# Performance work log

Hardware: AMD Instinct MI355X
Metric: run time of the kernel (lower is better)

## Reference

```python
import jax, jax.numpy as jnp
import numpy as np

HEADS = 8
HEAD_DIM = 48
INNER = HEADS * HEAD_DIM  # 384
GROUPS = 32
EPS = 1e-5
SCALE = HEAD_DIM ** -0.5


def group_norm(x, w, b):
    # x: [B,C,H,W]; GroupNorm(32, C) as in diffusion-style normalization()
    B, C, H, W = x.shape
    xg = x.reshape(B, GROUPS, C // GROUPS, H, W)
    mu = xg.mean(axis=(2, 3, 4), keepdims=True)
    var = xg.var(axis=(2, 3, 4), keepdims=True)
    xg = (xg - mu) * jax.lax.rsqrt(var + EPS)
    return xg.reshape(B, C, H, W) * w[None, :, None, None] + b[None, :, None, None]


def conv1x1(x, w, b):
    # 1x1 conv == per-pixel linear: w [Cout,Cin], x [B,Cin,H,W]
    return jnp.einsum('oc,bchw->bohw', w, x) + b[None, :, None, None]


def to_heads(t):
    # [B, INNER, H, W] -> [B, heads, H*W, head_dim]
    B, C, H, W = t.shape
    return t.reshape(B, HEADS, HEAD_DIM, H * W).transpose(0, 1, 3, 2)


def setup_inputs() -> dict:
    key = jax.random.key(0)
    ks = jax.random.split(key, 8)
    B, Cq, H, W = 4, 256, 48, 48
    return {
        'q_feat': jax.random.normal(ks[0], (B, Cq, H, W), jnp.float32),
        'kv_feat': jax.random.normal(ks[1], (B, Cq, H, W), jnp.float32),
        'gn_w': jnp.ones((Cq,), jnp.float32),
        'gn_b': jnp.zeros((Cq,), jnp.float32),
        'wq': jax.random.normal(ks[2], (INNER, Cq), jnp.float32) * 0.02,
        'bq': jnp.zeros((INNER,), jnp.float32),
        'wk': jax.random.normal(ks[3], (INNER, Cq), jnp.float32) * 0.02,
        'bk': jnp.zeros((INNER,), jnp.float32),
        'wv': jax.random.normal(ks[4], (INNER, Cq), jnp.float32) * 0.02,
        'bv': jnp.zeros((INNER,), jnp.float32),
        'wo': jax.random.normal(ks[5], (Cq, INNER), jnp.float32) * 0.02,
        'bo': jnp.zeros((Cq,), jnp.float32),
    }


def reference(q_feat, kv_feat, gn_w, gn_b, wq, bq, wk, bk, wv, bv, wo, bo):
    B, Cq, H, W = q_feat.shape
    q = conv1x1(group_norm(q_feat, gn_w, gn_b), wq, bq)
    k = conv1x1(kv_feat, wk, bk)  # kv_norm is Identity
    v = conv1x1(kv_feat, wv, bv)
    qh, kh, vh = to_heads(q), to_heads(k), to_heads(v)  # [B,h,N,d]
    scores = jnp.einsum('bhnd,bhmd->bhnm', qh, kh) * SCALE  # [B,h,N,N]
    attn = jax.nn.softmax(scores, axis=-1)
    o = jnp.einsum('bhnm,bhmd->bhnd', attn, vh)  # [B,h,N,d]
    o = o.transpose(0, 1, 3, 2).reshape(B, INNER, H, W)
    return conv1x1(o, wo, bo) + q_feat
```

## Files before the change

kernel.cpp:

```cpp
#include <hip/hip_runtime.h>
#include <hip/hip_bf16.h>

#define N_PIX 2304
#define C_IN  256
#define INNER 384
#define HEADS 8
#define HDIM  48
#define DPAD  64
#define QSCALE (0.14433756729740643f * 1.44269504088896341f)

typedef __bf16 bf16x8 __attribute__((ext_vector_type(8)));
typedef float  f32x4  __attribute__((ext_vector_type(4)));
typedef short  s16x8  __attribute__((ext_vector_type(8)));

union Frag { s16x8 s; bf16x8 b; uint2 u[2]; };

__device__ inline short f2bf_bits(float f){
  union { float f; unsigned u; } v; v.f = f;
  unsigned r = v.u + 0x7fffu + ((v.u >> 16) & 1u);
  return (short)(r >> 16);
}

__device__ inline unsigned cvt_pk(float a, float b){
  unsigned r; asm("v_cvt_pk_bf16_f32 %0, %1, %2" : "=v"(r) : "v"(a), "v"(b));
  return r;
}

__global__ __launch_bounds__(256) void gn_stats(const float* __restrict__ x,
                                                float* __restrict__ mu,
                                                float* __restrict__ rs){
  int bg = blockIdx.x;
  const float* p = x + (size_t)bg * 8 * N_PIX;
  float s = 0.f, s2 = 0.f;
  for (int i = threadIdx.x; i < 8 * N_PIX; i += 256){
    float v = p[i]; s += v; s2 += v * v;
  }
  __shared__ float ls[256], ls2[256];
  ls[threadIdx.x] = s; ls2[threadIdx.x] = s2;
  __syncthreads();
  for (int off = 128; off > 0; off >>= 1){
    if ((int)threadIdx.x < off){ ls[threadIdx.x] += ls[threadIdx.x + off]; ls2[threadIdx.x] += ls2[threadIdx.x + off]; }
    __syncthreads();
  }
  if (threadIdx.x == 0){
    float m = ls[0] / 18432.f;
    float var = ls2[0] / 18432.f - m * m;
    mu[bg] = m; rs[bg] = rsqrtf(var + 1e-5f);
  }
}

__global__ __launch_bounds__(256) void wconv(const float* __restrict__ a, const float* __restrict__ b,
                                             const float* __restrict__ c, const float* __restrict__ d,
                                             short* __restrict__ dst){
  int i = (blockIdx.x * 256 + threadIdx.x) * 8;
  const float* src;
  if (i < 98304) src = a + i;
  else if (i < 196608) src = b + (i - 98304);
  else if (i < 294912) src = c + (i - 196608);
  else src = d + (i - 294912);
  float4 v0 = *(const float4*)src;
  float4 v1 = *(const float4*)(src + 4);
  uint4 o;
  o.x = cvt_pk(v0.x, v0.y); o.y = cvt_pk(v0.z, v0.w);
  o.z = cvt_pk(v1.x, v1.y); o.w = cvt_pk(v1.z, v1.w);
  *(uint4*)(dst + i) = o;
}

__global__ __launch_bounds__(256) void prep_x(const float* __restrict__ Xq, const float* __restrict__ Xkv,
                                              const float* __restrict__ gnw, const float* __restrict__ gnb,
                                              const float* __restrict__ mu, const float* __restrict__ rs,
                                              short* __restrict__ XTq, short* __restrict__ XTkv){
  int which = blockIdx.z >> 2;
  int b = blockIdx.z & 3;
  int nb = blockIdx.x * 64, cb = blockIdx.y * 64;
  const float* X = which ? Xkv : Xq;
  short* XT = which ? XTkv : XTq;
  __shared__ __align__(16) short lt[64][68];
  int t = threadIdx.x;
  int c_l = t >> 4, n4 = (t & 15) * 4;
  #pragma unroll
  for (int i = 0; i < 4; ++i){
    int cl = c_l + i * 16, c = cb + cl;
    float4 v = *(const float4*)(X + ((size_t)b * C_IN + c) * N_PIX + nb + n4);
    if (which == 0){
      int bg = b * 32 + (c >> 3);
      float w = gnw[c] * rs[bg], bb = gnb[c] - mu[bg] * w;
      v.x = v.x * w + bb; v.y = v.y * w + bb; v.z = v.z * w + bb; v.w = v.w * w + bb;
    }
    uint2 p; p.x = cvt_pk(v.x, v.y); p.y = cvt_pk(v.z, v.w);
    *(uint2*)&lt[cl][n4] = p;
  }
  __syncthreads();
  #pragma unroll
  for (int i = 0; i < 2; ++i){
    int idx = t + i * 256;
    int n = idx >> 3, c8 = (idx & 7) * 8;
    s16x8 o;
    #pragma unroll
    for (int j = 0; j < 8; ++j) o[j] = lt[c8 + j][n];
    *(s16x8*)(XT + ((size_t)b * N_PIX + nb + n) * C_IN + cb + c8) = o;
  }
}

__global__ __launch_bounds__(256) void proj_qk(const short* __restrict__ XT,
                                               const short* __restrict__ WB,
                                               const float* __restrict__ bias,
                                               short* __restrict__ OUT, float scale){
  int b = blockIdx.z, nb = blockIdx.x * 64, ob = blockIdx.y * 64;
  int wave = threadIdx.x >> 6, lane = threadIdx.x & 63;
  int l16 = lane & 15, lq = lane >> 4;
  int o0 = ob + wave * 16;

  f32x4 acc[4] = {};
  const short* xbase = XT + ((size_t)b * N_PIX + nb) * C_IN;
  #pragma unroll
  for (int k = 0; k < 8; ++k){
    Frag wf; wf.s = *(const s16x8*)(WB + (size_t)(o0 + l16) * C_IN + k * 32 + lq * 8);
    #pragma unroll
    for (int nt = 0; nt < 4; ++nt){
      Frag af; af.s = *(const s16x8*)(xbase + (size_t)(nt * 16 + l16) * C_IN + k * 32 + lq * 8);
      acc[nt] = __builtin_amdgcn_mfma_f32_16x16x32_bf16(af.b, wf.b, acc[nt], 0, 0, 0);
    }
  }
  int o = o0 + l16;
  int h = (o * 683) >> 15, d = o - h * 48;
  float bv = bias[o];
  #pragma unroll
  for (int nt = 0; nt < 4; ++nt)
    #pragma unroll
    for (int r = 0; r < 4; ++r){
      int n = nb + nt * 16 + lq * 4 + r;
      OUT[(((size_t)b * HEADS + h) * N_PIX + n) * DPAD + d] = f2bf_bits((acc[nt][r] + bv) * scale);
    }

  if (ob == 0){
    s16x8 z = {0,0,0,0,0,0,0,0};
    for (int i = threadIdx.x; i < 1024; i += 256){
      int n = nb + (i >> 4);
      int hh = (i >> 1) & 7;
      int dd = 48 + (i & 1) * 8;
      *(s16x8*)(OUT + (((size_t)b * HEADS + hh) * N_PIX + n) * DPAD + dd) = z;
    }
  }
}

__global__ __launch_bounds__(256) void proj_v(const short* __restrict__ XT,
                                              const short* __restrict__ WB,
                                              const float* __restrict__ bias,
                                              short* __restrict__ VT){
  int b = blockIdx.z, nb = blockIdx.x * 64, ob = blockIdx.y * 64;
  int wave = threadIdx.x >> 6, lane = threadIdx.x & 63;
  int l16 = lane & 15, lq = lane >> 4;
  int o0 = ob + wave * 16;

  f32x4 acc[4] = {};
  const short* xbase = XT + ((size_t)b * N_PIX + nb) * C_IN;
  #pragma unroll
  for (int k = 0; k < 8; ++k){
    Frag wf; wf.s = *(const s16x8*)(WB + (size_t)(o0 + l16) * C_IN + k * 32 + lq * 8);
    #pragma unroll
    for (int nt = 0; nt < 4; ++nt){
      Frag xf; xf.s = *(const s16x8*)(xbase + (size_t)(nt * 16 + l16) * C_IN + k * 32 + lq * 8);
      acc[nt] = __builtin_amdgcn_mfma_f32_16x16x32_bf16(wf.b, xf.b, acc[nt], 0, 0, 0);
    }
  }
  #pragma unroll
  for (int r = 0; r < 4; ++r){
    int o = o0 + lq * 4 + r;
    int h = (o * 683) >> 15, d = o - h * 48;
    float bv = bias[o];
    #pragma unroll
    for (int nt = 0; nt < 4; ++nt){
      int n = nb + nt * 16 + l16;
      VT[(((size_t)b * HEADS + h) * DPAD + d) * N_PIX + n] = f2bf_bits(acc[nt][r] + bv);
    }
  }
}

__global__ __launch_bounds__(256) void attn_kernel(const short* __restrict__ Q,
                                                   const short* __restrict__ K,
                                                   const short* __restrict__ VT,
                                                   short* __restrict__ AOUT){
  int bh = blockIdx.y;
  int b = bh >> 3, h = bh & 7;
  int ib = blockIdx.x * 64;
  int wave = threadIdx.x >> 6, lane = threadIdx.x & 63;
  int l16 = lane & 15, lq = lane >> 4;
  int q0 = ib + wave * 16;

  __shared__ __align__(16) short kt[64 * 64];
  __shared__ __align__(16) short vt[64 * 64];
  __shared__ __align__(16) short pt[4][16 * 64];

  Frag qf[2];
  {
    const short* qp = Q + ((size_t)bh * N_PIX + q0 + l16) * DPAD + lq * 8;
    qf[0].s = *(const s16x8*)(qp);
    qf[1].s = *(const s16x8*)(qp + 32);
  }

  float m = -1e30f, l = 0.f;
  f32x4 oacc[3] = {};
  short* pw = &pt[wave][0];

  for (int jt = 0; jt < N_PIX / 64; ++jt){
    __syncthreads();
    #pragma unroll
    for (int it = 0; it < 2; ++it){
      int idx = threadIdx.x + it * 256;
      int row = idx >> 3, cb = idx & 7;
      int scb = cb ^ (row & 7);
      *(s16x8*)(kt + row * 64 + scb * 8) =
        *(const s16x8*)(K + ((size_t)bh * N_PIX + jt * 64 + row) * DPAD + cb * 8);
      *(s16x8*)(vt + row * 64 + scb * 8) =
        *(const s16x8*)(VT + ((size_t)bh * DPAD + row) * N_PIX + jt * 64 + cb * 8);
    }
    __syncthreads();

    f32x4 sc[4] = {};
    #pragma unroll
    for (int ct = 0; ct < 4; ++ct){
      int jr = ct * 16 + l16;
      #pragma unroll
      for (int kk = 0; kk < 2; ++kk){
        Frag kf;
        kf.s = *(const s16x8*)(kt + jr * 64 + ((kk * 4 + lq) ^ (jr & 7)) * 8);
        sc[ct] = __builtin_amdgcn_mfma_f32_16x16x32_bf16(kf.b, qf[kk].b, sc[ct], 0, 0, 0);
      }
    }

    float mx = fmaxf(
      fmaxf(fmaxf(fmaxf(sc[0][0], sc[0][1]), fmaxf(sc[0][2], sc[0][3])),
            fmaxf(fmaxf(sc[1][0], sc[1][1]), fmaxf(sc[1][2], sc[1][3]))),
      fmaxf(fmaxf(fmaxf(sc[2][0], sc[2][1]), fmaxf(sc[2][2], sc[2][3])),
            fmaxf(fmaxf(sc[3][0], sc[3][1]), fmaxf(sc[3][2], sc[3][3]))));
    mx = fmaxf(mx, __shfl_xor(mx, 16));
    mx = fmaxf(mx, __shfl_xor(mx, 32));
    float mnew = fmaxf(m, mx);
    float corr = __builtin_amdgcn_exp2f(m - mnew);
    m = mnew;
    float ps = 0.f;
    #pragma unroll
    for (int ct = 0; ct < 4; ++ct)
      #pragma unroll
      for (int r = 0; r < 4; ++r){
        float p = __builtin_amdgcn_exp2f(sc[ct][r] - mnew);
        sc[ct][r] = p; ps += p;
      }
    ps += __shfl_xor(ps, 16);
    ps += __shfl_xor(ps, 32);
    l = l * corr + ps;
    #pragma unroll
    for (int dt = 0; dt < 3; ++dt)
      #pragma unroll
      for (int r = 0; r < 4; ++r) oacc[dt][r] *= corr;

    #pragma unroll
    for (int ct = 0; ct < 4; ++ct){
      uint2 p; p.x = cvt_pk(sc[ct][0], sc[ct][1]); p.y = cvt_pk(sc[ct][2], sc[ct][3]);
      *(uint2*)(pw + l16 * 64 + (((ct * 4 + lq) ^ l16) * 4)) = p;
    }

    #pragma unroll
    for (int kk = 0; kk < 2; ++kk){
      Frag pf;
      pf.u[0] = *(const uint2*)(pw + l16 * 64 + ((((kk * 8 + lq * 2)    ) ^ l16) * 4));
      pf.u[1] = *(const uint2*)(pw + l16 * 64 + ((((kk * 8 + lq * 2) + 1) ^ l16) * 4));
      #pragma unroll
      for (int dt = 0; dt < 3; ++dt){
        int vr = dt * 16 + l16;
        Frag vf;
        vf.s = *(const s16x8*)(vt + vr * 64 + ((kk * 4 + lq) ^ (vr & 7)) * 8);
        oacc[dt] = __builtin_amdgcn_mfma_f32_16x16x32_bf16(vf.b, pf.b, oacc[dt], 0, 0, 0);
      }
    }
  }

  float inv = 1.f / l;
  short* op = AOUT + ((size_t)b * N_PIX + q0 + l16) * INNER + h * HDIM + lq * 4;
  #pragma unroll
  for (int dt = 0; dt < 3; ++dt){
    uint2 w;
    w.x = cvt_pk(oacc[dt][0] * inv, oacc[dt][1] * inv);
    w.y = cvt_pk(oacc[dt][2] * inv, oacc[dt][3] * inv);
    *(uint2*)(op + dt * 16) = w;
  }
}

__global__ __launch_bounds__(256) void proj_o(const short* __restrict__ WOB,
                                              const float* __restrict__ BO,
                                              const short* __restrict__ AOUT,
                                              const float* __restrict__ RES,
                                              float* __restrict__ OUT){
  int b = blockIdx.z, nb = blockIdx.x * 64, ob = blockIdx.y * 64;
  int wave = threadIdx.x >> 6, lane = threadIdx.x & 63;
  int l16 = lane & 15, lq = lane >> 4;
  int o0 = ob + wave * 16;

  f32x4 acc[4] = {};
  const short* abase = AOUT + ((size_t)b * N_PIX + nb) * INNER;
  #pragma unroll
  for (int k = 0; k < 12; ++k){
    Frag wf; wf.s = *(const s16x8*)(WOB + (size_t)(o0 + l16) * INNER + k * 32 + lq * 8);
    #pragma unroll
    for (int nt = 0; nt < 4; ++nt){
      Frag af; af.s = *(const s16x8*)(abase + (size_t)(nt * 16 + l16) * INNER + k * 32 + lq * 8);
      acc[nt] = __builtin_amdgcn_mfma_f32_16x16x32_bf16(wf.b, af.b, acc[nt], 0, 0, 0);
    }
  }
  #pragma unroll
  for (int r = 0; r < 4; ++r){
    int o = o0 + lq * 4 + r;
    float bv = BO[o];
    #pragma unroll
    for (int nt = 0; nt < 4; ++nt){
      int n = nb + nt * 16 + l16;
      size_t idx = ((size_t)b * C_IN + o) * N_PIX + n;
      OUT[idx] = acc[nt][r] + bv + RES[idx];
    }
  }
}

extern "C" void kernel_launch(void* const* d_in, const int* in_sizes, int n_in,
                              void* d_out, int out_size, void* d_ws, size_t ws_size,
                              hipStream_t stream){
  const float* q_feat = (const float*)d_in[0];
  const float* kv_feat= (const float*)d_in[1];
  const float* gn_w   = (const float*)d_in[2];
  const float* gn_b   = (const float*)d_in[3];
  const float* wq     = (const float*)d_in[4];
  const float* bq     = (const float*)d_in[5];
  const float* wk     = (const float*)d_in[6];
  const float* bk     = (const float*)d_in[7];
  const float* wv     = (const float*)d_in[8];
  const float* bv     = (const float*)d_in[9];
  const float* wo     = (const float*)d_in[10];
  const float* bo     = (const float*)d_in[11];
  float* out = (float*)d_out;

  char* ws = (char*)d_ws;
  float* mu = (float*)ws;
  float* rs = (float*)(ws + 512);
  short* wbf  = (short*)(ws + 4096);
  short* xtq  = (short*)(ws + 790528);
  short* xtkv = (short*)(ws + 5509120);
  short* qh   = (short*)(ws + 10227712);
  short* kh   = (short*)(ws + 19664896);
  short* vtb  = (short*)(ws + 29102080);
  short* aout = (short*)(ws + 790528);

  gn_stats<<<128, 256, 0, stream>>>(q_feat, mu, rs);
  wconv<<<192, 256, 0, stream>>>(wq, wk, wv, wo, wbf);
  prep_x<<<dim3(36, 4, 8), 256, 0, stream>>>(q_feat, kv_feat, gn_w, gn_b, mu, rs, xtq, xtkv);

  proj_qk<<<dim3(36, 6, 4), 256, 0, stream>>>(xtq,  wbf,          bq, qh, (float)QSCALE);
  proj_qk<<<dim3(36, 6, 4), 256, 0, stream>>>(xtkv, wbf + 98304,  bk, kh, 1.0f);
  proj_v <<<dim3(36, 6, 4), 256, 0, stream>>>(xtkv, wbf + 196608, bv, vtb);

  attn_kernel<<<dim3(36, 32), 256, 0, stream>>>(qh, kh, vtb, aout);

  proj_o<<<dim3(36, 4, 4), 256, 0, stream>>>(wbf + 294912, bo, aout, q_feat, out);
}
```

Before: 290.6 us.

## Merge launches, double K/V tile size with register prefetch, lazy softmax rescale

Merges gn_stats with wconv and the three QKV projections into single launches to cut launch overhead. The attention kernel now works on 128-key tiles, prefetches the next K/V tile into registers while computing the current one, and remaps blocks so that the 8 heads sharing a batch are scheduled together. It also skips the online-softmax rescale unless the running max grows by more than a threshold. These changes raise LDS and register use per block, which may lower occupancy.

```diff
diff --git a/kernel.cpp b/kernel.cpp
--- a/kernel.cpp
+++ b/kernel.cpp
@@ -26,44 +26,44 @@
   return r;
 }
 
-__global__ __launch_bounds__(256) void gn_stats(const float* __restrict__ x,
-                                                float* __restrict__ mu,
-                                                float* __restrict__ rs){
-  int bg = blockIdx.x;
-  const float* p = x + (size_t)bg * 8 * N_PIX;
-  float s = 0.f, s2 = 0.f;
-  for (int i = threadIdx.x; i < 8 * N_PIX; i += 256){
-    float v = p[i]; s += v; s2 += v * v;
-  }
+__global__ __launch_bounds__(256) void gn_wconv(const float* __restrict__ x,
+                                                float* __restrict__ mu, float* __restrict__ rs,
+                                                const float* __restrict__ wa, const float* __restrict__ wb,
+                                                const float* __restrict__ wc, const float* __restrict__ wd,
+                                                short* __restrict__ dst){
   __shared__ float ls[256], ls2[256];
-  ls[threadIdx.x] = s; ls2[threadIdx.x] = s2;
-  __syncthreads();
-  for (int off = 128; off > 0; off >>= 1){
-    if ((int)threadIdx.x < off){ ls[threadIdx.x] += ls[threadIdx.x + off]; ls2[threadIdx.x] += ls2[threadIdx.x + off]; }
+  if (blockIdx.x < 128){
+    int bg = blockIdx.x;
+    const float* p = x + (size_t)bg * 8 * N_PIX;
+    float s = 0.f, s2 = 0.f;
+    for (int i = threadIdx.x; i < 8 * N_PIX; i += 256){
+      float v = p[i]; s += v; s2 += v * v;
+    }
+    ls[threadIdx.x] = s; ls2[threadIdx.x] = s2;
     __syncthreads();
-  }
-  if (threadIdx.x == 0){
-    float m = ls[0] / 18432.f;
-    float var = ls2[0] / 18432.f - m * m;
-    mu[bg] = m; rs[bg] = rsqrtf(var + 1e-5f);
-  }
-}
-
-__global__ __launch_bounds__(256) void wconv(const float* __restrict__ a, const float* __restrict__ b,
-                                             const float* __restrict__ c, const float* __restrict__ d,
-                                             short* __restrict__ dst){
-  int i = (blockIdx.x * 256 + threadIdx.x) * 8;
-  const float* src;
-  if (i < 98304) src = a + i;
-  else if (i < 196608) src = b + (i - 98304);
-  else if (i < 294912) src = c + (i - 196608);
-  else src = d + (i - 294912);
-  float4 v0 = *(const float4*)src;
-  float4 v1 = *(const float4*)(src + 4);
-  uint4 o;
-  o.x = cvt_pk(v0.x, v0.y); o.y = cvt_pk(v0.z, v0.w);
-  o.z = cvt_pk(v1.x, v1.y); o.w = cvt_pk(v1.z, v1.w);
-  *(uint4*)(dst + i) = o;
+    for (int off = 128; off > 0; off >>= 1){
+      if ((int)threadIdx.x < off){ ls[threadIdx.x] += ls[threadIdx.x + off]; ls2[threadIdx.x] += ls2[threadIdx.x + off]; }
+      __syncthreads();
+    }
+    if (threadIdx.x == 0){
+      float m = ls[0] / 18432.f;
+      float var = ls2[0] / 18432.f - m * m;
+      mu[bg] = m; rs[bg] = rsqrtf(var + 1e-5f);
+    }
+  } else {
+    int i = ((blockIdx.x - 128) * 256 + threadIdx.x) * 8;
+    const float* src;
+    if (i < 98304) src = wa + i;
+    else if (i < 196608) src = wb + (i - 98304);
+    else if (i < 294912) src = wc + (i - 196608);
+    else src = wd + (i - 294912);
+    float4 v0 = *(const float4*)src;
+    float4 v1 = *(const float4*)(src + 4);
+    uint4 o;
+    o.x = cvt_pk(v0.x, v0.y); o.y = cvt_pk(v0.z, v0.w);
+    o.z = cvt_pk(v1.x, v1.y); o.w = cvt_pk(v1.z, v1.w);
+    *(uint4*)(dst + i) = o;
+  }
 }
 
 __global__ __launch_bounds__(256) void prep_x(const float* __restrict__ Xq, const float* __restrict__ Xkv,
@@ -102,11 +102,21 @@
   }
 }
 
-__global__ __launch_bounds__(256) void proj_qk(const short* __restrict__ XT,
-                                               const short* __restrict__ WB,
-                                               const float* __restrict__ bias,
-                                               short* __restrict__ OUT, float scale){
-  int b = blockIdx.z, nb = blockIdx.x * 64, ob = blockIdx.y * 64;
+__global__ __launch_bounds__(256) void proj_qkv(const short* __restrict__ XTq,
+                                                const short* __restrict__ XTkv,
+                                                const short* __restrict__ WBF,
+                                                const float* __restrict__ bq,
+                                                const float* __restrict__ bk,
+                                                const float* __restrict__ bv,
+                                                short* __restrict__ QH,
+                                                short* __restrict__ KH,
+                                                short* __restrict__ VTB){
+  int b = blockIdx.z, nb = blockIdx.x * 64;
+  int y = blockIdx.y;
+  int which = y / 6;
+  int ob = (y % 6) * 64;
+  const short* XT = which ? XTkv : XTq;
+  const short* WB = WBF + which * 98304;
   int wave = threadIdx.x >> 6, lane = threadIdx.x & 63;
   int l16 = lane & 15, lq = lane >> 4;
   int o0 = ob + wave * 16;
@@ -119,60 +129,45 @@
     #pragma unroll
     for (int nt = 0; nt < 4; ++nt){
       Frag af; af.s = *(const s16x8*)(xbase + (size_t)(nt * 16 + l16) * C_IN + k * 32 + lq * 8);
-      acc[nt] = __builtin_amdgcn_mfma_f32_16x16x32_bf16(af.b, wf.b, acc[nt], 0, 0, 0);
-    }
-  }
-  int o = o0 + l16;
-  int h = (o * 683) >> 15, d = o - h * 48;
-  float bv = bias[o];
-  #pragma unroll
-  for (int nt = 0; nt < 4; ++nt)
+      acc[nt] = (which == 2)
+        ? __builtin_amdgcn_mfma_f32_16x16x32_bf16(wf.b, af.b, acc[nt], 0, 0, 0)
+        : __builtin_amdgcn_mfma_f32_16x16x32_bf16(af.b, wf.b, acc[nt], 0, 0, 0);
+  }
+  }
+  if (which == 2){
     #pragma unroll
     for (int r = 0; r < 4; ++r){
-      int n = nb + nt * 16 + lq * 4 + r;
-      OUT[(((size_t)b * HEADS + h) * N_PIX + n) * DPAD + d] = f2bf_bits((acc[nt][r] + bv) * scale);
-    }
-
-  if (ob == 0){
-    s16x8 z = {0,0,0,0,0,0,0,0};
-    for (int i = threadIdx.x; i < 1024; i += 256){
-      int n = nb + (i >> 4);
-      int hh = (i >> 1) & 7;
-      int dd = 48 + (i & 1) * 8;
-      *(s16x8*)(OUT + (((size_t)b * HEADS + hh) * N_PIX + n) * DPAD + dd) = z;
-    }
-  }
-}
-
-__global__ __launch_bounds__(256) void proj_v(const short* __restrict__ XT,
-                                              const short* __restrict__ WB,
-                                              const float* __restrict__ bias,
-                                              short* __restrict__ VT){
-  int b = blockIdx.z, nb = blockIdx.x * 64, ob = blockIdx.y * 64;
-  int wave = threadIdx.x >> 6, lane = threadIdx.x & 63;
-  int l16 = lane & 15, lq = lane >> 4;
-  int o0 = ob + wave * 16;
-
-  f32x4 acc[4] = {};
-  const short* xbase = XT + ((size_t)b * N_PIX + nb) * C_IN;
-  #pragma unroll
-  for (int k = 0; k < 8; ++k){
-    Frag wf; wf.s = *(const s16x8*)(WB + (size_t)(o0 + l16) * C_IN + k * 32 + lq * 8);
-    #pragma unroll
-    for (int nt = 0; nt < 4; ++nt){
-      Frag xf; xf.s = *(const s16x8*)(xbase + (size_t)(nt * 16 + l16) * C_IN + k * 32 + lq * 8);
-      acc[nt] = __builtin_amdgcn_mfma_f32_16x16x32_bf16(wf.b, xf.b, acc[nt], 0, 0, 0);
-    }
-  }
-  #pragma unroll
-  for (int r = 0; r < 4; ++r){
-    int o = o0 + lq * 4 + r;
+      int o = o0 + lq * 4 + r;
+      int h = (o * 683) >> 15, d = o - h * 48;
+      float bvv = bv[o];
+      #pragma unroll
+      for (int nt = 0; nt < 4; ++nt){
+        int n = nb + nt * 16 + l16;
+        VTB[(((size_t)b * HEADS + h) * DPAD + d) * N_PIX + n] = f2bf_bits(acc[nt][r] + bvv);
+      }
+    }
+  } else {
+    short* OUT = which ? KH : QH;
+    const float* bias = which ? bk : bq;
+    float scale = which ? 1.0f : (float)QSCALE;
+    int o = o0 + l16;
     int h = (o * 683) >> 15, d = o - h * 48;
-    float bv = bias[o];
-    #pragma unroll
-    for (int nt = 0; nt < 4; ++nt){
-      int n = nb + nt * 16 + l16;
-      VT[(((size_t)b * HEADS + h) * DPAD + d) * N_PIX + n] = f2bf_bits(acc[nt][r] + bv);
+    float bvv = bias[o];
+    #pragma unroll
+    for (int nt = 0; nt < 4; ++nt)
+      #pragma unroll
+      for (int r = 0; r < 4; ++r){
+        int n = nb + nt * 16 + lq * 4 + r;
+        OUT[(((size_t)b * HEADS + h) * N_PIX + n) * DPAD + d] = f2bf_bits((acc[nt][r] + bvv) * scale);
+      }
+    if (which == 0 && ob == 0){
+      s16x8 z = {0,0,0,0,0,0,0,0};
+      for (int i = threadIdx.x; i < 1024; i += 256){
+        int n = nb + (i >> 4);
+        int hh = (i >> 1) & 7;
+        int dd = 48 + (i & 1) * 8;
+        *(s16x8*)(QH + (((size_t)b * HEADS + hh) * N_PIX + n) * DPAD + dd) = z;
+      }
     }
   }
 }
@@ -181,16 +176,26 @@
                                                    const short* __restrict__ K,
                                                    const short* __restrict__ VT,
                                                    short* __restrict__ AOUT){
-  int bh = blockIdx.y;
+  int f = blockIdx.x;
+  int t = f >> 3;
+  int ib = (t % 36) * 64;
+  int bh = (f & 7) + 8 * (t / 36);
   int b = bh >> 3, h = bh & 7;
-  int ib = blockIdx.x * 64;
-  int wave = threadIdx.x >> 6, lane = threadIdx.x & 63;
+  int tid = threadIdx.x;
+  int wave = tid >> 6, lane = tid & 63;
   int l16 = lane & 15, lq = lane >> 4;
   int q0 = ib + wave * 16;
 
-  __shared__ __align__(16) short kt[64 * 64];
-  __shared__ __align__(16) short vt[64 * 64];
-  __shared__ __align__(16) short pt[4][16 * 64];
+  __shared__ __align__(16) short kt[128 * 64];
+  __shared__ __align__(16) short vt[64 * 128];
+  __shared__ __align__(16) short pt[4][16 * 132];
+
+  int kr = tid >> 3, kc = tid & 7;
+  int ksw = (kc ^ (kr & 7)) * 8;
+  int vr = tid >> 4, vc = tid & 15;
+  int vsw = (vc ^ (vr & 7)) * 8;
+  const short* kbase = K + (size_t)bh * N_PIX * DPAD;
+  const short* vbase = VT + (size_t)bh * DPAD * N_PIX;
 
   Frag qf[2];
   {
@@ -199,27 +204,39 @@
     qf[1].s = *(const s16x8*)(qp + 32);
   }
 
+  Frag kst[4], vst[4];
+  #pragma unroll
+  for (int it = 0; it < 4; ++it){
+    kst[it].s = *(const s16x8*)(kbase + (size_t)(kr + it * 32) * DPAD + kc * 8);
+    vst[it].s = *(const s16x8*)(vbase + (size_t)(vr + it * 16) * N_PIX + vc * 8);
+  }
+
   float m = -1e30f, l = 0.f;
   f32x4 oacc[3] = {};
   short* pw = &pt[wave][0];
 
-  for (int jt = 0; jt < N_PIX / 64; ++jt){
+  for (int jt = 0; jt < N_PIX / 128; ++jt){
     __syncthreads();
     #pragma unroll
-    for (int it = 0; it < 2; ++it){
-      int idx = threadIdx.x + it * 256;
-      int row = idx >> 3, cb = idx & 7;
-      int scb = cb ^ (row & 7);
-      *(s16x8*)(kt + row * 64 + scb * 8) =
-        *(const s16x8*)(K + ((size_t)bh * N_PIX + jt * 64 + row) * DPAD + cb * 8);
-      *(s16x8*)(vt + row * 64 + scb * 8) =
-        *(const s16x8*)(VT + ((size_t)bh * DPAD + row) * N_PIX + jt * 64 + cb * 8);
+    for (int it = 0; it < 4; ++it){
+      *(s16x8*)(kt + (kr + it * 32) * 64 + ksw) = kst[it].s;
+      *(s16x8*)(vt + (vr + it * 16) * 128 + vsw) = vst[it].s;
+    }
+    if (jt < N_PIX / 128 - 1){
+      const short* kb2 = kbase + (size_t)(jt + 1) * 128 * DPAD;
+      const short* vb2 = vbase + (jt + 1) * 128;
+      #pragma unroll
+      for (int it = 0; it < 4; ++it){
+        kst[it].s = *(const s16x8*)(kb2 + (size_t)(kr + it * 32) * DPAD + kc * 8);
+        vst[it].s = *(const s16x8*)(vb2 + (size_t)(vr + it * 16) * N_PIX + vc * 8);
+      }
     }
     __syncthreads();
 
-    f32x4 sc[4] = {};
-    #pragma unroll
-    for (int ct = 0; ct < 4; ++ct){
+    f32x4 sc[8];
+    #pragma unroll
+    for (int ct = 0; ct < 8; ++ct){
+      sc[ct] = (f32x4){0.f, 0.f, 0.f, 0.f};
       int jr = ct * 16 + l16;
       #pragma unroll
       for (int kk = 0; kk < 2; ++kk){
@@ -229,48 +246,51 @@
       }
     }
 
-    float mx = fmaxf(
-      fmaxf(fmaxf(fmaxf(sc[0][0], sc[0][1]), fmaxf(sc[0][2], sc[0][3])),
-            fmaxf(fmaxf(sc[1][0], sc[1][1]), fmaxf(sc[1][2], sc[1][3]))),
-      fmaxf(fmaxf(fmaxf(sc[2][0], sc[2][1]), fmaxf(sc[2][2], sc[2][3])),
-            fmaxf(fmaxf(sc[3][0], sc[3][1]), fmaxf(sc[3][2], sc[3][3]))));
+    float mx = sc[0][0];
+    #pragma unroll
+    for (int ct = 0; ct < 8; ++ct)
+      #pragma unroll
+      for (int r = 0; r < 4; ++r) mx = fmaxf(mx, sc[ct][r]);
     mx = fmaxf(mx, __shfl_xor(mx, 16));
     mx = fmaxf(mx, __shfl_xor(mx, 32));
-    float mnew = fmaxf(m, mx);
-    float corr = __builtin_amdgcn_exp2f(m - mnew);
-    m = mnew;
+    if (!__all(mx <= m + 8.f)){
+      float mnew = fmaxf(m, mx);
+      float corr = __builtin_amdgcn_exp2f(m - mnew);
+      m = mnew;
+      l *= corr;
+      #pragma unroll
+      for (int dt = 0; dt < 3; ++dt)
+        #pragma unroll
+        for (int r = 0; r < 4; ++r) oacc[dt][r] *= corr;
+    }
     float ps = 0.f;
     #pragma unroll
-    for (int ct = 0; ct < 4; ++ct)
+    for (int ct = 0; ct < 8; ++ct)
       #pragma unroll
       for (int r = 0; r < 4; ++r){
-        float p = __builtin_amdgcn_exp2f(sc[ct][r] - mnew);
+        float p = __builtin_amdgcn_exp2f(sc[ct][r] - m);
         sc[ct][r] = p; ps += p;
       }
     ps += __shfl_xor(ps, 16);
     ps += __shfl_xor(ps, 32);
-    l = l * corr + ps;
-    #pragma unroll
-    for (int dt = 0; dt < 3; ++dt)
-      #pragma unroll
-      for (int r = 0; r < 4; ++r) oacc[dt][r] *= corr;
-
-    #pragma unroll
-    for (int ct = 0; ct < 4; ++ct){
+    l += ps;
+
+    #pragma unroll
+    for (int ct = 0; ct < 8; ++ct){
       uint2 p; p.x = cvt_pk(sc[ct][0], sc[ct][1]); p.y = cvt_pk(sc[ct][2], sc[ct][3]);
-      *(uint2*)(pw + l16 * 64 + (((ct * 4 + lq) ^ l16) * 4)) = p;
-    }
-
-    #pragma unroll
-    for (int kk = 0; kk < 2; ++kk){
+      *(uint2*)(pw + l16 * 132 + (((ct * 4 + lq) ^ l16) * 4)) = p;
+    }
+
+    #pragma unroll
+    for (int kk = 0; kk < 4; ++kk){
       Frag pf;
-      pf.u[0] = *(const uint2*)(pw + l16 * 64 + ((((kk * 8 + lq * 2)    ) ^ l16) * 4));
-      pf.u[1] = *(const uint2*)(pw + l16 * 64 + ((((kk * 8 + lq * 2) + 1) ^ l16) * 4));
+      pf.u[0] = *(const uint2*)(pw + l16 * 132 + ((((kk * 8 + lq * 2)    ) ^ l16) * 4));
+      pf.u[1] = *(const uint2*)(pw + l16 * 132 + ((((kk * 8 + lq * 2) + 1) ^ l16) * 4));
       #pragma unroll
       for (int dt = 0; dt < 3; ++dt){
-        int vr = dt * 16 + l16;
+        int vrr = dt * 16 + l16;
         Frag vf;
-        vf.s = *(const s16x8*)(vt + vr * 64 + ((kk * 4 + lq) ^ (vr & 7)) * 8);
+        vf.s = *(const s16x8*)(vt + vrr * 128 + ((kk * 4 + lq) ^ (vrr & 7)) * 8);
         oacc[dt] = __builtin_amdgcn_mfma_f32_16x16x32_bf16(vf.b, pf.b, oacc[dt], 0, 0, 0);
       }
     }
@@ -349,15 +369,9 @@
   short* vtb  = (short*)(ws + 29102080);
   short* aout = (short*)(ws + 790528);
 
-  gn_stats<<<128, 256, 0, stream>>>(q_feat, mu, rs);
-  wconv<<<192, 256, 0, stream>>>(wq, wk, wv, wo, wbf);
+  gn_wconv<<<320, 256, 0, stream>>>(q_feat, mu, rs, wq, wk, wv, wo, wbf);
   prep_x<<<dim3(36, 4, 8), 256, 0, stream>>>(q_feat, kv_feat, gn_w, gn_b, mu, rs, xtq, xtkv);
-
-  proj_qk<<<dim3(36, 6, 4), 256, 0, stream>>>(xtq,  wbf,          bq, qh, (float)QSCALE);
-  proj_qk<<<dim3(36, 6, 4), 256, 0, stream>>>(xtkv, wbf + 98304,  bk, kh, 1.0f);
-  proj_v <<<dim3(36, 6, 4), 256, 0, stream>>>(xtkv, wbf + 196608, bv, vtb);
-
-  attn_kernel<<<dim3(36, 32), 256, 0, stream>>>(qh, kh, vtb, aout);
-
+  proj_qkv<<<dim3(36, 18, 4), 256, 0, stream>>>(xtq, xtkv, wbf, bq, bk, bv, qh, kh, vtb);
+  attn_kernel<<<1152, 256, 0, stream>>>(qh, kh, vtb, aout);
   proj_o<<<dim3(36, 4, 4), 256, 0, stream>>>(wbf + 294912, bo, aout, q_feat, out);
 }
```

After: 315.8 us. 8.7% more time.
